# Performance work log

Measured on AMD Instinct MI355X. Metric: run time of the kernel, lower is better.

Reference implementation:

```python
import jax, jax.numpy as jnp
import numpy as np

C_CODE, F_OUT, K_TOP, M_GRP, GROUPS, STRIDE, KSZ = 64, 256, 4, 8, 8, 4, 4
B, W, H = 4, 64, 64


def setup_inputs() -> dict:
    key = jax.random.key(0)
    k1, k2, k3, k4, k5 = jax.random.split(key, 5)
    shape = (B, K_TOP, M_GRP, W, H)
    ind_pos = jax.random.randint(k1, shape, 0, C_CODE, dtype=jnp.int32)
    ind_neg = jax.random.randint(k2, shape, 0, C_CODE, dtype=jnp.int32)
    val_pos = jax.random.normal(k3, shape, dtype=jnp.float32)
    val_neg = jax.random.normal(k4, shape, dtype=jnp.float32)
    # torch conv_transpose2d weight layout: [Cin, Cout/groups, kh, kw]
    weight = jax.random.normal(k5, (C_CODE * M_GRP, F_OUT // GROUPS, KSZ, KSZ), dtype=jnp.float32) * 0.05
    return {"ind_pos": ind_pos, "ind_neg": ind_neg, "val_pos": val_pos, "val_neg": val_neg, "weight": weight}


def _deindex_and_deconv(ind_pos, ind_neg, val_pos, val_neg, weight):
    b, k, m, w, h = ind_pos.shape
    c = C_CODE
    # offset each m-group's indices into the flattened c*m channel axis
    offs = (c * jnp.arange(m, dtype=jnp.int32)).reshape(1, 1, m, 1, 1)
    ip = (ind_pos + offs).reshape(b, k * m, w, h)
    iN = (ind_neg + offs).reshape(b, k * m, w, h)
    vp = val_pos.reshape(b, k * m, w, h)
    vn = val_neg.reshape(b, k * m, w, h)
    bb = jnp.arange(b).reshape(b, 1, 1, 1)
    ww = jnp.arange(w).reshape(1, 1, w, 1)
    hh = jnp.arange(h).reshape(1, 1, 1, h)
    out = jnp.zeros((b, c * m, w, h), dtype=vp.dtype)
    out = out.at[bb, ip, ww, hh].set(vp)  # scatter pos values along channel dim
    out = out.at[bb, iN, ww, hh].set(vn)  # neg scatter second (overwrites ties, like torch)
    # conv_transpose2d(stride=STRIDE, padding=0, groups=GROUPS) as dilated conv:
    # rearrange torch weight [Cin, Cout/g, kh, kw] -> OIHW [Cout, Cin/g, kh, kw], flip spatial
    cin, cog, kh, kw = weight.shape
    g = GROUPS
    rhs = weight.reshape(g, cin // g, cog, kh, kw).transpose(0, 2, 1, 3, 4).reshape(g * cog, cin // g, kh, kw)
    rhs = rhs[:, :, ::-1, ::-1]
    y = jax.lax.conv_general_dilated(
        out, rhs,
        window_strides=(1, 1),
        padding=[(kh - 1, kh - 1), (kw - 1, kw - 1)],
        lhs_dilation=(STRIDE, STRIDE),
        dimension_numbers=("NCHW", "OIHW", "NCHW"),
        feature_group_count=g,
    )
    return y


def reference(ind_pos, ind_neg, val_pos, val_neg, weight):
    return _deindex_and_deconv(ind_pos, ind_neg, val_pos, val_neg, weight)
```

## Files before the change

### kernel.cpp

```cpp
#include <hip/hip_runtime.h>


typedef float f32x4  __attribute__((ext_vector_type(4)));
typedef short bf16x8 __attribute__((ext_vector_type(8)));

__device__ __forceinline__ unsigned short f32_to_bf16_rne(float f) {
    unsigned int u = __float_as_uint(f);
    return (unsigned short)((u + 0x7FFFu + ((u >> 16) & 1u)) >> 16);
}

__global__ __launch_bounds__(256) void wt_transpose_kernel(
    const float* __restrict__ weight, unsigned short* __restrict__ ws)
{
    __shared__ unsigned short stile[64 * 72];
    const int m    = blockIdx.x >> 3;
    const int pblk = blockIdx.x & 7;
    const int t    = threadIdx.x;
    const int p    = t & 63;
    const int chi  = t >> 6;
    #pragma unroll
    for (int r = 0; r < 16; ++r) {
        const int c = chi * 16 + r;
        const float v = weight[(size_t)(64 * m + c) * 512 + pblk * 64 + p];
        stile[p * 72 + c] = f32_to_bf16_rne(v);
    }
    __syncthreads();
    uint4* dst4 = (uint4*)(ws + (size_t)(m * 512 + pblk * 64) * 64);
    #pragma unroll
    for (int pass = 0; pass < 2; ++pass) {
        const int g = pass * 256 + t;
        const uint4 v = *(const uint4*)(stile + (g >> 3) * 72 + (g & 7) * 8);
        dst4[g] = v;
    }
}

__global__ __launch_bounds__(256) void convdeidx_mfma_kernel(
    const int* __restrict__ ind_pos, const int* __restrict__ ind_neg,
    const float* __restrict__ val_pos, const float* __restrict__ val_neg,
    const unsigned short* __restrict__ ws, float* __restrict__ out)
{
    __shared__ unsigned short sA[256 * 72];
    __shared__ unsigned short sX[4 * 64 * 72];

    const int bi  = blockIdx.x;
    const int wg  = bi & 15;
    const int m   = (bi >> 4) & 7;
    const int b   = bi >> 7;
    const int w0  = wg * 4;
    const int tid = threadIdx.x;
    const int wid = tid >> 6, lane = tid & 63;
    const int q   = lane >> 4, ln = lane & 15;

    const int wl = tid >> 6;
    const int h  = tid & 63;
    int   ipos[4], ineg[4];
    float vpos[4], vneg[4];
    #pragma unroll
    for (int k = 0; k < 4; ++k) {
        const size_t idx = ((((size_t)b * 4 + k) * 8 + m) * 64 + (w0 + wl)) * 64 + h;
        ipos[k] = ind_pos[idx]; vpos[k] = val_pos[idx];
        ineg[k] = ind_neg[idx]; vneg[k] = val_neg[idx];
    }

    {
        uint4* x4 = (uint4*)sX;
        const uint4 z = make_uint4(0u, 0u, 0u, 0u);
        #pragma unroll
        for (int r = 0; r < 9; ++r) x4[r * 256 + tid] = z;
    }

    const uint4* wsrc4 = (const uint4*)(ws + (size_t)m * 512 * 64);
    #pragma unroll
    for (int r = 0; r < 8; ++r) {
        const int g = r * 256 + tid;
        const uint4 v = wsrc4[g];
        *(uint4*)(sA + (g >> 3) * 72 + (g & 7) * 8) = v;
    }
    __syncthreads();

    {
        unsigned short* xrow = sX + (wl * 64 + h) * 72;
        #pragma unroll
        for (int k = 0; k < 4; ++k) xrow[ipos[k]] = f32_to_bf16_rne(vpos[k]);
        #pragma unroll
        for (int k = 0; k < 4; ++k) xrow[ineg[k]] = f32_to_bf16_rne(vneg[k]);
    }
    __syncthreads();

    f32x4* outv = (f32x4*)out;

    #pragma unroll
    for (int chunk = 0; chunk < 2; ++chunk) {
        if (chunk == 1) {
            __syncthreads();
            #pragma unroll
            for (int r = 0; r < 8; ++r) {
                const int g = r * 256 + tid;
                const uint4 v = wsrc4[2048 + g];
                *(uint4*)(sA + (g >> 3) * 72 + (g & 7) * 8) = v;
            }
            __syncthreads();
        }

        bf16x8 afr[2][4];
        #pragma unroll
        for (int kt = 0; kt < 2; ++kt)
            #pragma unroll
            for (int mt = 0; mt < 4; ++mt)
                afr[kt][mt] = *(const bf16x8*)(sA + (wid * 64 + mt * 16 + ln) * 72 + (kt * 4 + q) * 8);

        const int ocg0 = chunk * 16 + wid * 4;

        #pragma unroll
        for (int ww = 0; ww < 4; ++ww) {
            bf16x8 bfr[2][4];
            #pragma unroll
            for (int kt = 0; kt < 2; ++kt)
                #pragma unroll
                for (int nt = 0; nt < 4; ++nt)
                    bfr[kt][nt] = *(const bf16x8*)(sX + (ww * 64 + nt * 16 + ln) * 72 + (kt * 4 + q) * 8);

            f32x4 acc[4][4];
            #pragma unroll
            for (int mt = 0; mt < 4; ++mt)
                #pragma unroll
                for (int nt = 0; nt < 4; ++nt)
                    acc[mt][nt] = (f32x4){0.f, 0.f, 0.f, 0.f};

            #pragma unroll
            for (int kt = 0; kt < 2; ++kt)
                #pragma unroll
                for (int mt = 0; mt < 4; ++mt)
                    #pragma unroll
                    for (int nt = 0; nt < 4; ++nt)
                        acc[mt][nt] = __builtin_amdgcn_mfma_f32_16x16x32_bf16(
                            afr[kt][mt], bfr[kt][nt], acc[mt][nt], 0, 0, 0);

            #pragma unroll
            for (int mt = 0; mt < 4; ++mt) {
                const size_t rowbase =
                    ((size_t)(b * 256 + m * 32 + ocg0 + mt) * 256 + ((w0 + ww) * 4 + q)) * 64;
                #pragma unroll
                for (int nt = 0; nt < 4; ++nt)
                    __builtin_nontemporal_store(acc[mt][nt], outv + rowbase + nt * 16 + ln);
            }
        }
    }
}

extern "C" void kernel_launch(void* const* d_in, const int* in_sizes, int n_in,
                              void* d_out, int out_size, void* d_ws, size_t ws_size,
                              hipStream_t stream) {
    const int*   ind_pos = (const int*)  d_in[0];
    const int*   ind_neg = (const int*)  d_in[1];
    const float* val_pos = (const float*)d_in[2];
    const float* val_neg = (const float*)d_in[3];
    const float* weight  = (const float*)d_in[4];
    float*       y       = (float*)d_out;
    unsigned short* ws   = (unsigned short*)d_ws;

    hipLaunchKernelGGL(wt_transpose_kernel, dim3(64), dim3(256), 0, stream, weight, ws);
    hipLaunchKernelGGL(convdeidx_mfma_kernel, dim3(512), dim3(256), 0, stream,
                       ind_pos, ind_neg, val_pos, val_neg, ws, y);
}
```

Measured before the change: 288.4 us.

## Drop weight LDS staging, halve w-tile per block, split N tiles for occupancy

Result: faster. 281.3 us (-2.5%).

```diff
diff --git a/kernel.cpp b/kernel.cpp
--- a/kernel.cpp
+++ b/kernel.cpp
@@ -34,51 +34,45 @@
     }
 }
 
-__global__ __launch_bounds__(256) void convdeidx_mfma_kernel(
+__global__ __launch_bounds__(256, 4) void convdeidx_mfma_kernel(
     const int* __restrict__ ind_pos, const int* __restrict__ ind_neg,
     const float* __restrict__ val_pos, const float* __restrict__ val_neg,
     const unsigned short* __restrict__ ws, float* __restrict__ out)
 {
-    __shared__ unsigned short sA[256 * 72];
-    __shared__ unsigned short sX[4 * 64 * 72];
+    __shared__ unsigned short sX[2 * 64 * 72];
 
     const int bi  = blockIdx.x;
-    const int wg  = bi & 15;
-    const int m   = (bi >> 4) & 7;
-    const int b   = bi >> 7;
-    const int w0  = wg * 4;
+    const int wg  = bi & 31;
+    const int m   = (bi >> 5) & 7;
+    const int b   = bi >> 8;
+    const int w0  = wg * 2;
     const int tid = threadIdx.x;
     const int wid = tid >> 6, lane = tid & 63;
     const int q   = lane >> 4, ln = lane & 15;
 
-    const int wl = tid >> 6;
-    const int h  = tid & 63;
     int   ipos[4], ineg[4];
     float vpos[4], vneg[4];
-    #pragma unroll
-    for (int k = 0; k < 4; ++k) {
-        const size_t idx = ((((size_t)b * 4 + k) * 8 + m) * 64 + (w0 + wl)) * 64 + h;
-        ipos[k] = ind_pos[idx]; vpos[k] = val_pos[idx];
-        ineg[k] = ind_neg[idx]; vneg[k] = val_neg[idx];
+    const int wl = (tid >> 6) & 1;
+    const int h  = tid & 63;
+    if (tid < 128) {
+        #pragma unroll
+        for (int k = 0; k < 4; ++k) {
+            const size_t idx = ((((size_t)b * 4 + k) * 8 + m) * 64 + (w0 + wl)) * 64 + h;
+            ipos[k] = ind_pos[idx]; vpos[k] = val_pos[idx];
+            ineg[k] = ind_neg[idx]; vneg[k] = val_neg[idx];
+        }
     }
 
     {
         uint4* x4 = (uint4*)sX;
         const uint4 z = make_uint4(0u, 0u, 0u, 0u);
         #pragma unroll
-        for (int r = 0; r < 9; ++r) x4[r * 256 + tid] = z;
-    }
-
-    const uint4* wsrc4 = (const uint4*)(ws + (size_t)m * 512 * 64);
-    #pragma unroll
-    for (int r = 0; r < 8; ++r) {
-        const int g = r * 256 + tid;
-        const uint4 v = wsrc4[g];
-        *(uint4*)(sA + (g >> 3) * 72 + (g & 7) * 8) = v;
+        for (int r = 0; r < 4; ++r) x4[r * 256 + tid] = z;
+        if (tid < 128) x4[1024 + tid] = z;
     }
     __syncthreads();
 
-    {
+    if (tid < 128) {
         unsigned short* xrow = sX + (wl * 64 + h) * 72;
         #pragma unroll
         for (int k = 0; k < 4; ++k) xrow[ipos[k]] = f32_to_bf16_rne(vpos[k]);
@@ -87,62 +81,58 @@
     }
     __syncthreads();
 
+    const unsigned short* wsm = ws + (size_t)m * 512 * 64;
     f32x4* outv = (f32x4*)out;
 
     #pragma unroll
     for (int chunk = 0; chunk < 2; ++chunk) {
-        if (chunk == 1) {
-            __syncthreads();
-            #pragma unroll
-            for (int r = 0; r < 8; ++r) {
-                const int g = r * 256 + tid;
-                const uint4 v = wsrc4[2048 + g];
-                *(uint4*)(sA + (g >> 3) * 72 + (g & 7) * 8) = v;
-            }
-            __syncthreads();
-        }
-
         bf16x8 afr[2][4];
         #pragma unroll
         for (int kt = 0; kt < 2; ++kt)
             #pragma unroll
             for (int mt = 0; mt < 4; ++mt)
-                afr[kt][mt] = *(const bf16x8*)(sA + (wid * 64 + mt * 16 + ln) * 72 + (kt * 4 + q) * 8);
+                afr[kt][mt] = *(const bf16x8*)(
+                    wsm + ((size_t)(chunk * 256 + wid * 64 + mt * 16 + ln) << 6) + (kt * 4 + q) * 8);
 
         const int ocg0 = chunk * 16 + wid * 4;
 
         #pragma unroll
-        for (int ww = 0; ww < 4; ++ww) {
-            bf16x8 bfr[2][4];
+        for (int ww = 0; ww < 2; ++ww) {
             #pragma unroll
-            for (int kt = 0; kt < 2; ++kt)
+            for (int nh = 0; nh < 2; ++nh) {
+                bf16x8 bfr[2][2];
                 #pragma unroll
-                for (int nt = 0; nt < 4; ++nt)
-                    bfr[kt][nt] = *(const bf16x8*)(sX + (ww * 64 + nt * 16 + ln) * 72 + (kt * 4 + q) * 8);
+                for (int kt = 0; kt < 2; ++kt)
+                    #pragma unroll
+                    for (int nt2 = 0; nt2 < 2; ++nt2)
+                        bfr[kt][nt2] = *(const bf16x8*)(
+                            sX + (ww * 64 + (nh * 2 + nt2) * 16 + ln) * 72 + (kt * 4 + q) * 8);
 
-            f32x4 acc[4][4];
-            #pragma unroll
-            for (int mt = 0; mt < 4; ++mt)
-                #pragma unroll
-                for (int nt = 0; nt < 4; ++nt)
-                    acc[mt][nt] = (f32x4){0.f, 0.f, 0.f, 0.f};
-
-            #pragma unroll
-            for (int kt = 0; kt < 2; ++kt)
+                f32x4 acc[4][2];
                 #pragma unroll
                 for (int mt = 0; mt < 4; ++mt)
                     #pragma unroll
-                    for (int nt = 0; nt < 4; ++nt)
-                        acc[mt][nt] = __builtin_amdgcn_mfma_f32_16x16x32_bf16(
-                            afr[kt][mt], bfr[kt][nt], acc[mt][nt], 0, 0, 0);
+                    for (int nt2 = 0; nt2 < 2; ++nt2)
+                        acc[mt][nt2] = (f32x4){0.f, 0.f, 0.f, 0.f};
 
-            #pragma unroll
-            for (int mt = 0; mt < 4; ++mt) {
-                const size_t rowbase =
-                    ((size_t)(b * 256 + m * 32 + ocg0 + mt) * 256 + ((w0 + ww) * 4 + q)) * 64;
                 #pragma unroll
-                for (int nt = 0; nt < 4; ++nt)
-                    __builtin_nontemporal_store(acc[mt][nt], outv + rowbase + nt * 16 + ln);
+                for (int kt = 0; kt < 2; ++kt)
+                    #pragma unroll
+                    for (int mt = 0; mt < 4; ++mt)
+                        #pragma unroll
+                        for (int nt2 = 0; nt2 < 2; ++nt2)
+                            acc[mt][nt2] = __builtin_amdgcn_mfma_f32_16x16x32_bf16(
+                                afr[kt][mt], bfr[kt][nt2], acc[mt][nt2], 0, 0, 0);
+
+                #pragma unroll
+                for (int mt = 0; mt < 4; ++mt) {
+                    const size_t rowbase =
+                        ((size_t)(b * 256 + m * 32 + ocg0 + mt) * 256 + ((w0 + ww) * 4 + q)) * 64;
+                    #pragma unroll
+                    for (int nt2 = 0; nt2 < 2; ++nt2)
+                        __builtin_nontemporal_store(
+                            acc[mt][nt2], outv + rowbase + (nh * 2 + nt2) * 16 + ln);
+                }
             }
         }
     }
@@ -160,6 +150,6 @@
     unsigned short* ws   = (unsigned short*)d_ws;
 
     hipLaunchKernelGGL(wt_transpose_kernel, dim3(64), dim3(256), 0, stream, weight, ws);
-    hipLaunchKernelGGL(convdeidx_mfma_kernel, dim3(512), dim3(256), 0, stream,
+    hipLaunchKernelGGL(convdeidx_mfma_kernel, dim3(1024), dim3(256), 0, stream,
                        ind_pos, ind_neg, val_pos, val_neg, ws, y);
 }
```
